# Kernel tuning notes

Measured on AMD Instinct MI355X. Metric: run time of the kernel, lower is better.

## Reference

```python
import jax, jax.numpy as jnp
import numpy as np

N_NODES = 20000
C_IN = 128
C_OUT = 128
C_MID = 8            # max(C_IN // 16, 8) per TP.__init__
NEIGHBOR_CG = 8
INF = 1000000.0
EPS = 1e-5
# real spherical harmonics for l=1 are ordered (m=-1,0,1) ~ (y,z,x)
P_L1 = jnp.array([[0., 1., 0.], [0., 0., 1.], [1., 0., 0.]], dtype=jnp.float32)


def equivariant_layer_norm(x, ln_w, ln_b):
    # x: (N, 4, C); l=0 block x[:, :1], l=1 block x[:, 1:4]
    x0 = x[:, :1, :]
    x0 = x0 - jnp.mean(x0, axis=-1, keepdims=True)          # mean only for l=0
    n0 = jnp.mean(jnp.sum(x0 * x0, axis=1, keepdims=True), axis=-1, keepdims=True)
    y0 = x0 * jax.lax.rsqrt(n0 + EPS) * ln_w[0] + ln_b
    x1 = x[:, 1:4, :]
    n1 = jnp.mean(jnp.sum(x1 * x1, axis=1, keepdims=True), axis=-1, keepdims=True)
    y1 = x1 * jax.lax.rsqrt(n1 + EPS) * ln_w[1]
    return jnp.concatenate([y0, y1], axis=1)


def rotation_to_z(vec):
    # vec: (..., 3) -> R with R @ unit(vec) = z_hat (Rodrigues, safe at c ~ -1)
    n = jnp.linalg.norm(vec, axis=-1, keepdims=True)
    v = vec / (n + 1e-9)
    c = v[..., 2]
    kx, ky = v[..., 1], -v[..., 0]                 # k = v x z_hat = (v_y, -v_x, 0)
    zero = jnp.zeros_like(kx)
    K = jnp.stack([
        jnp.stack([zero, zero, ky], -1),
        jnp.stack([zero, zero, -kx], -1),
        jnp.stack([-ky, kx, zero], -1)], -2)
    safe = c > -0.999
    denom = jnp.where(safe, 1.0 + c, 1.0)
    I = jnp.eye(3, dtype=vec.dtype)
    R = I + K + jnp.matmul(K, K) / denom[..., None, None]
    flip = jnp.array([[1., 0., 0.], [0., -1., 0.], [0., 0., -1.]], dtype=vec.dtype)
    return jnp.where(safe[..., None, None], R, flip)


def escn_tensor_product(msg, vec, so2_w0, so2_wr, so2_wi):
    # msg: (N, H, 4, Cm), vec: (N, H, 3)
    R = rotation_to_z(vec)                                      # (N,H,3,3)
    D1 = jnp.einsum('ij,nhjk,lk->nhil', P_L1, R, P_L1)          # Wigner-D, l=1
    l1 = jnp.einsum('nhij,nhjc->nhic', D1, msg[..., 1:4, :])    # rotate to edge frame
    # m = 0 channel mix across degrees (l=0 coeff, l=1 m=0 coeff)
    m0_in = jnp.stack([msg[..., 0, :], l1[..., 1, :]], axis=-2)  # (N,H,2,Cm)
    m0 = (m0_in.reshape(m0_in.shape[:-2] + (2 * C_MID,)) @ so2_w0).reshape(m0_in.shape)
    # m = +/-1 SO(2) convolution
    x_m1, x_p1 = l1[..., 0, :], l1[..., 2, :]
    y_p1 = x_p1 @ so2_wr - x_m1 @ so2_wi
    y_m1 = x_m1 @ so2_wr + x_p1 @ so2_wi
    out_l1 = jnp.stack([y_m1, m0[..., 1, :], y_p1], axis=-2)     # (N,H,3,Cm)
    out_l1 = jnp.einsum('nhji,nhjc->nhic', D1, out_l1)           # rotate back (D1^T)
    return jnp.concatenate([m0[..., :1, :], out_l1], axis=-2)    # (N,H,4,Cm)


def setup_inputs() -> dict:
    key = jax.random.key(0)
    ks = jax.random.split(key, 10)
    s_feats = jax.random.normal(ks[0], (N_NODES, 4, C_IN), jnp.float32)
    s_points = jax.random.normal(ks[1], (N_NODES, 3), jnp.float32) * 5.0
    neighbor_indices = jax.random.randint(ks[2], (N_NODES, 9), 0, N_NODES + 1)
    ln_w = 1.0 + 0.02 * jax.random.normal(ks[3], (2, C_IN), jnp.float32)
    ln_b = 0.02 * jax.random.normal(ks[4], (C_IN,), jnp.float32)
    w_in = jax.random.normal(ks[5], (2 * C_IN, C_MID), jnp.float32) / np.sqrt(2 * C_IN)
    w_out = jax.random.normal(ks[6], (C_MID, C_OUT), jnp.float32) / np.sqrt(C_MID)
    so2_w0 = jax.random.normal(ks[7], (2 * C_MID, 2 * C_MID), jnp.float32) / np.sqrt(2 * C_MID)
    so2_wr = jax.random.normal(ks[8], (C_MID, C_MID), jnp.float32) / np.sqrt(C_MID)
    so2_wi = jax.random.normal(ks[9], (C_MID, C_MID), jnp.float32) / np.sqrt(C_MID)
    return dict(s_feats=s_feats, s_points=s_points, neighbor_indices=neighbor_indices,
                ln_w=ln_w, ln_b=ln_b, w_in=w_in, w_out=w_out,
                so2_w0=so2_w0, so2_wr=so2_wr, so2_wi=so2_wi)


def reference(s_feats, s_points, neighbor_indices, ln_w, ln_b, w_in, w_out, so2_w0, so2_wr, so2_wi):
    N = s_feats.shape[0]
    x = equivariant_layer_norm(s_feats, ln_w, ln_b)                  # (N,4,C)
    sp_pad = jnp.concatenate([s_points, jnp.full((1, 3), INF, s_points.dtype)], 0)
    x_pad = jnp.concatenate([x, jnp.zeros_like(x[:1])], 0)
    idx = neighbor_indices[:, 1:]                                     # drop self
    mask = (idx < N).astype(x.dtype)                                  # (N,Hfull)
    npts = (sp_pad[idx] * mask[..., None])[:, :NEIGHBOR_CG]           # (N,H,3)
    nfts = (x_pad[idx] * mask[..., None, None])[:, :NEIGHBOR_CG]      # (N,H,4,C)
    vec = npts - s_points[:, None, :]                                 # (N,H,3)
    sfe = jnp.broadcast_to(x[:, None], nfts.shape)                    # (N,H,4,C)
    msg = jnp.concatenate([nfts, sfe], axis=-1) @ w_in                # (N,H,4,Cm)
    msg = escn_tensor_product(msg, vec, so2_w0, so2_wr, so2_wi)       # (N,H,4,Cm)
    out = msg.sum(axis=1) @ w_out                                     # (N,4,C_out)
    return out
```

## Files before the change

### kernel.cpp

```cpp
#include <hip/hip_runtime.h>
#include <math.h>

typedef float fx4 __attribute__((ext_vector_type(4)));
typedef float fx2 __attribute__((ext_vector_type(2)));

#define SWZ8(x)  __int_as_float(__builtin_amdgcn_ds_swizzle(__float_as_int(x), 0x201F))
#define SWZ16(x) __int_as_float(__builtin_amdgcn_ds_swizzle(__float_as_int(x), 0x401F))
#define SX32(x)  __shfl_xor((x), 32)

__global__ __launch_bounds__(256, 4) void k1_ln_proj(
    const float* __restrict__ s_feats,
    const float* __restrict__ ln_w,
    const float* __restrict__ ln_b,
    const float* __restrict__ w_in,
    float* __restrict__ ys,
    int N)
{
    const int lane = threadIdx.x & 63;
    const int kq = lane & 7;
    const int cg = lane >> 3;
    const int n = blockIdx.x * 4 + (threadIdx.x >> 6);

    float wa0[16], wa1[16], wb0[16], wb1[16];
    float B1 = 0.f, C1 = 0.f, B2 = 0.f, C2 = 0.f;
    #pragma unroll
    for (int t = 0; t < 16; t++) {
        int c = cg * 16 + t;
        float w1 = w_in[c * 8 + kq];
        float w2 = w_in[(128 + c) * 8 + kq];
        float l0 = ln_w[c], l1 = ln_w[128 + c], lb = ln_b[c];
        wa0[t] = w1 * l0; wa1[t] = w1 * l1;
        wb0[t] = w2 * l0; wb1[t] = w2 * l1;
        B1 += w1 * l0; C1 += lb * w1;
        B2 += w2 * l0; C2 += lb * w2;
    }
    B1 += SWZ8(B1);  C1 += SWZ8(C1);  B2 += SWZ8(B2);  C2 += SWZ8(C2);
    B1 += SWZ16(B1); C1 += SWZ16(C1); B2 += SWZ16(B2); C2 += SWZ16(C2);
    B1 += SX32(B1);  C1 += SX32(C1);  B2 += SX32(B2);  C2 += SX32(C2);

    if (n >= N) return;

    const float* sp = s_feats + (size_t)n * 512 + cg * 16;
    float accY[4] = {0.f, 0.f, 0.f, 0.f};
    float accS[4] = {0.f, 0.f, 0.f, 0.f};
    float ssum = 0.f, sq0 = 0.f, sq1 = 0.f;
    #pragma unroll
    for (int m = 0; m < 4; m++) {
        #pragma unroll
        for (int i = 0; i < 4; i++) {
            fx4 v = __builtin_nontemporal_load((const fx4*)(sp + m * 128 + i * 4));
            float e0 = v.x, e1 = v.y, e2 = v.z, e3 = v.w;
            if (m == 0) {
                accY[0] += e0 * wa0[i*4+0] + e1 * wa0[i*4+1] + e2 * wa0[i*4+2] + e3 * wa0[i*4+3];
                accS[0] += e0 * wb0[i*4+0] + e1 * wb0[i*4+1] + e2 * wb0[i*4+2] + e3 * wb0[i*4+3];
                ssum += e0 + e1 + e2 + e3;
                sq0  += e0 * e0 + e1 * e1 + e2 * e2 + e3 * e3;
            } else {
                accY[m] += e0 * wa1[i*4+0] + e1 * wa1[i*4+1] + e2 * wa1[i*4+2] + e3 * wa1[i*4+3];
                accS[m] += e0 * wb1[i*4+0] + e1 * wb1[i*4+1] + e2 * wb1[i*4+2] + e3 * wb1[i*4+3];
                sq1  += e0 * e0 + e1 * e1 + e2 * e2 + e3 * e3;
            }
        }
    }
    #define RED_ALL(FN) \
        accY[0] += FN(accY[0]); accY[1] += FN(accY[1]); accY[2] += FN(accY[2]); accY[3] += FN(accY[3]); \
        accS[0] += FN(accS[0]); accS[1] += FN(accS[1]); accS[2] += FN(accS[2]); accS[3] += FN(accS[3]); \
        ssum += FN(ssum); sq0 += FN(sq0); sq1 += FN(sq1);
    RED_ALL(SWZ8)
    RED_ALL(SWZ16)
    RED_ALL(SX32)
    #undef RED_ALL

    float mean = ssum * (1.0f / 128.0f);
    float r0 = rsqrtf((sq0 - ssum * mean) * (1.0f / 128.0f) + 1e-5f);
    float r1 = rsqrtf(sq1 * (1.0f / 128.0f) + 1e-5f);

    float aA = (cg & 2) ? ((cg & 1) ? accY[3] : accY[2]) : ((cg & 1) ? accY[1] : accY[0]);
    float aB = (cg & 2) ? ((cg & 1) ? accS[3] : accS[2]) : ((cg & 1) ? accS[1] : accS[0]);
    float av = (cg & 4) ? aB : aA;
    float Bv = (cg & 4) ? B2 : B1;
    float Cv = (cg & 4) ? C2 : C1;
    bool isM0 = (cg & 3) == 0;
    float outv = isM0 ? (r0 * (av - mean * Bv) + Cv) : (r1 * av);

    int src = ((lane >> 2) & 7) + ((lane & 3) << 3) + (lane & 32);
    float myv = __shfl(outv, src);
    ys[(size_t)n * 64 + lane] = myv;
}

#define TROW 40

__global__ __launch_bounds__(256, 4) void k2_edges(
    const float* __restrict__ ys,
    const float* __restrict__ s_points,
    const int*   __restrict__ nbr,
    const float* __restrict__ w0,
    const float* __restrict__ wr,
    const float* __restrict__ wi,
    const float* __restrict__ w_out,
    float* __restrict__ out,
    int N)
{
    __shared__ float tbuf[8][8 * TROW];
    __shared__ float abuf[8][32];

    const int tid = threadIdx.x;
    const int lane = tid & 63;
    const int h = lane >> 3, k = lane & 7;
    const int wv = tid >> 6;
    const int base = (blockIdx.x * 4 + wv) * 2;

    float c00[8], c08[8], c10[8], c18[8], cwr[8], cwi[8];
    #pragma unroll
    for (int j = 0; j < 8; j++) {
        c00[j] = w0[j * 16 + k];
        c08[j] = w0[(8 + j) * 16 + k];
        c10[j] = w0[j * 16 + 8 + k];
        c18[j] = w0[(8 + j) * 16 + 8 + k];
        cwr[j] = wr[j * 8 + k];
        cwi[j] = wi[j * 8 + k];
    }
    float wc0[8], wc1[8];
    #pragma unroll
    for (int kk = 0; kk < 8; kk++) {
        fx2 w2v = *(const fx2*)&w_out[kk * 128 + lane * 2];
        wc0[kk] = w2v.x; wc1[kk] = w2v.y;
    }

    if (base >= N) return;
    const int n1 = base + 1;
    const bool v1 = n1 < N;

    int idx0 = nbr[base * 9 + 1 + h];
    int idx1 = v1 ? nbr[n1 * 9 + 1 + h] : 0x7fffffff;
    bool mk0 = idx0 < N, mk1 = idx1 < N;

    float px0 = s_points[base * 3], py0 = s_points[base * 3 + 1], pz0 = s_points[base * 3 + 2];
    float px1 = v1 ? s_points[n1 * 3]     : 0.f;
    float py1 = v1 ? s_points[n1 * 3 + 1] : 0.f;
    float pz1 = v1 ? s_points[n1 * 3 + 2] : 0.f;
    float nx0 = mk0 ? s_points[idx0 * 3]     : 0.f;
    float ny0 = mk0 ? s_points[idx0 * 3 + 1] : 0.f;
    float nz0 = mk0 ? s_points[idx0 * 3 + 2] : 0.f;
    float nx1 = mk1 ? s_points[idx1 * 3]     : 0.f;
    float ny1 = mk1 ? s_points[idx1 * 3 + 1] : 0.f;
    float nz1 = mk1 ? s_points[idx1 * 3 + 2] : 0.f;
    fx4 yv0 = mk0 ? *(const fx4*)(ys + (size_t)idx0 * 64 + k * 4) : (fx4){0.f,0.f,0.f,0.f};
    fx4 yv1 = mk1 ? *(const fx4*)(ys + (size_t)idx1 * 64 + k * 4) : (fx4){0.f,0.f,0.f,0.f};
    fx4 sv0 = *(const fx4*)(ys + (size_t)base * 64 + 32 + k * 4);
    fx4 sv1 = v1 ? *(const fx4*)(ys + (size_t)n1 * 64 + 32 + k * 4) : (fx4){0.f,0.f,0.f,0.f};

    auto node_compute = [&](int slot, int nn, float PX, float PY, float PZ,
                            float NX, float NY, float NZ, fx4 YV, fx4 SV) {
        float vx = NX - PX, vy = NY - PY, vz = NZ - PZ;
        float nrm = sqrtf(vx * vx + vy * vy + vz * vz);
        float inv = 1.0f / (nrm + 1e-9f);
        float ux = vx * inv, uy = vy * inv, uz = vz * inv;
        float cz = uz;
        float kx = uy, ky = -ux;
        bool safe = cz > -0.999f;
        float idd = safe ? 1.0f / (1.0f + cz) : 1.0f;
        float D00, D01, D02, D10, D11, D12, D20, D21, D22;
        {
            float R00, R01, R02, R10, R11, R12, R20, R21, R22;
            if (safe) {
                R00 = 1.0f - ky * ky * idd; R01 = kx * ky * idd;        R02 = ky;
                R10 = kx * ky * idd;        R11 = 1.0f - kx * kx * idd; R12 = -kx;
                R20 = -ky;                  R21 = kx;                   R22 = 1.0f - (kx * kx + ky * ky) * idd;
            } else {
                R00 = 1.0f; R01 = 0.0f; R02 = 0.0f;
                R10 = 0.0f; R11 = -1.0f; R12 = 0.0f;
                R20 = 0.0f; R21 = 0.0f; R22 = -1.0f;
            }
            D00 = R11; D01 = R12; D02 = R10;
            D10 = R21; D11 = R22; D12 = R20;
            D20 = R01; D21 = R02; D22 = R00;
        }
        float msg0 = YV.x + SV.x, msg1 = YV.y + SV.y, msg2 = YV.z + SV.z, msg3 = YV.w + SV.w;
        float l1_0 = D00 * msg1 + D01 * msg2 + D02 * msg3;
        float l1_1 = D10 * msg1 + D11 * msg2 + D12 * msg3;
        float l1_2 = D20 * msg1 + D21 * msg2 + D22 * msg3;

        *(fx4*)&tbuf[slot][h * TROW + k * 4] = (fx4){msg0, l1_0, l1_1, l1_2};

        float m00 = 0.f, m01 = 0.f, ypl = 0.f, yml = 0.f;
        #pragma unroll
        for (int j = 0; j < 8; j++) {
            fx4 t = *(const fx4*)&tbuf[slot][h * TROW + j * 4];
            m00 += t.x * c00[j] + t.z * c08[j];
            m01 += t.x * c10[j] + t.z * c18[j];
            ypl += t.w * cwr[j] - t.y * cwi[j];
            yml += t.y * cwr[j] + t.w * cwi[j];
        }
        float f0 = m00;
        float f1 = D00 * yml + D10 * m01 + D20 * ypl;
        float f2 = D01 * yml + D11 * m01 + D21 * ypl;
        float f3 = D02 * yml + D12 * m01 + D22 * ypl;

        f0 += SWZ8(f0);  f1 += SWZ8(f1);  f2 += SWZ8(f2);  f3 += SWZ8(f3);
        f0 += SWZ16(f0); f1 += SWZ16(f1); f2 += SWZ16(f2); f3 += SWZ16(f3);
        f0 += SX32(f0);  f1 += SX32(f1);  f2 += SX32(f2);  f3 += SX32(f3);

        if (h == 0)
            *(fx4*)&abuf[slot][k * 4] = (fx4){f0, f1, f2, f3};

        float o0[4] = {0.f, 0.f, 0.f, 0.f}, o1[4] = {0.f, 0.f, 0.f, 0.f};
        #pragma unroll
        for (int kk = 0; kk < 8; kk++) {
            fx4 a = *(const fx4*)&abuf[slot][kk * 4];
            o0[0] += a.x * wc0[kk]; o1[0] += a.x * wc1[kk];
            o0[1] += a.y * wc0[kk]; o1[1] += a.y * wc1[kk];
            o0[2] += a.z * wc0[kk]; o1[2] += a.z * wc1[kk];
            o0[3] += a.w * wc0[kk]; o1[3] += a.w * wc1[kk];
        }
        float* op = out + (size_t)nn * 512;
        #pragma unroll
        for (int m = 0; m < 4; m++)
            *(fx2*)(op + m * 128 + lane * 2) = (fx2){o0[m], o1[m]};
    };

    node_compute(wv * 2 + 0, base, px0, py0, pz0, nx0, ny0, nz0, yv0, sv0);
    if (v1)
        node_compute(wv * 2 + 1, n1, px1, py1, pz1, nx1, ny1, nz1, yv1, sv1);
}

extern "C" void kernel_launch(void* const* d_in, const int* in_sizes, int n_in,
                              void* d_out, int out_size, void* d_ws, size_t ws_size,
                              hipStream_t stream) {
    const float* s_feats  = (const float*)d_in[0];
    const float* s_points = (const float*)d_in[1];
    const int*   nbr      = (const int*)d_in[2];
    const float* ln_w     = (const float*)d_in[3];
    const float* ln_b     = (const float*)d_in[4];
    const float* w_in     = (const float*)d_in[5];
    const float* w_out    = (const float*)d_in[6];
    const float* so2_w0   = (const float*)d_in[7];
    const float* so2_wr   = (const float*)d_in[8];
    const float* so2_wi   = (const float*)d_in[9];
    float* out = (float*)d_out;

    int N = in_sizes[0] / 512;
    float* ys = (float*)d_ws;

    int nb1 = (N + 3) / 4;
    int nb2 = (N + 7) / 8;
    k1_ln_proj<<<nb1, 256, 0, stream>>>(s_feats, ln_w, ln_b, w_in, ys, N);
    k2_edges<<<nb2, 256, 0, stream>>>(ys, s_points, nbr, so2_w0, so2_wr, so2_wi,
                                      w_out, out, N);
}
```

Before: 68.10 us.

## Process multiple nodes per wave in both kernels and vectorize output stores

Each wave in the layer-norm/projection kernel now handles five nodes, and each wave in the edge kernel handles eight nodes in pairs. The weight setup (w_in products and reductions, SO(2) and w_out weights) is amortized over more work and far fewer blocks are launched. The edge kernel loads w_out as fx4 and writes output with 128-bit stores split across half-waves. The first reduction step moves from a ds_swizzle to a DPP row operation. The trade-offs are fewer waves to hide gather latency and a lower occupancy hint on the edge kernel.

```diff
diff --git a/kernel.cpp b/kernel.cpp
--- a/kernel.cpp
+++ b/kernel.cpp
@@ -4,9 +4,15 @@
 typedef float fx4 __attribute__((ext_vector_type(4)));
 typedef float fx2 __attribute__((ext_vector_type(2)));
 
-#define SWZ8(x)  __int_as_float(__builtin_amdgcn_ds_swizzle(__float_as_int(x), 0x201F))
+__device__ __forceinline__ float DPP8(float x) {
+    int t = __builtin_amdgcn_update_dpp(0, __float_as_int(x), 0x128, 0xf, 0xf, false);
+    return __int_as_float(t);
+}
 #define SWZ16(x) __int_as_float(__builtin_amdgcn_ds_swizzle(__float_as_int(x), 0x401F))
 #define SX32(x)  __shfl_xor((x), 32)
+
+#define K1_NPW 5
+#define K2_NPW 8
 
 __global__ __launch_bounds__(256, 4) void k1_ln_proj(
     const float* __restrict__ s_feats,
@@ -19,7 +25,7 @@
     const int lane = threadIdx.x & 63;
     const int kq = lane & 7;
     const int cg = lane >> 3;
-    const int n = blockIdx.x * 4 + (threadIdx.x >> 6);
+    const int w = blockIdx.x * 4 + (threadIdx.x >> 6);
 
     float wa0[16], wa1[16], wb0[16], wb1[16];
     float B1 = 0.f, C1 = 0.f, B2 = 0.f, C2 = 0.f;
@@ -34,63 +40,68 @@
         B1 += w1 * l0; C1 += lb * w1;
         B2 += w2 * l0; C2 += lb * w2;
     }
-    B1 += SWZ8(B1);  C1 += SWZ8(C1);  B2 += SWZ8(B2);  C2 += SWZ8(C2);
+    B1 += DPP8(B1);  C1 += DPP8(C1);  B2 += DPP8(B2);  C2 += DPP8(C2);
     B1 += SWZ16(B1); C1 += SWZ16(C1); B2 += SWZ16(B2); C2 += SWZ16(C2);
     B1 += SX32(B1);  C1 += SX32(C1);  B2 += SX32(B2);  C2 += SX32(C2);
 
-    if (n >= N) return;
-
-    const float* sp = s_feats + (size_t)n * 512 + cg * 16;
-    float accY[4] = {0.f, 0.f, 0.f, 0.f};
-    float accS[4] = {0.f, 0.f, 0.f, 0.f};
-    float ssum = 0.f, sq0 = 0.f, sq1 = 0.f;
-    #pragma unroll
-    for (int m = 0; m < 4; m++) {
+    const int n0 = w * K1_NPW;
+    const int src = ((lane >> 2) & 7) + ((lane & 3) << 3) + (lane & 32);
+
+    #pragma unroll
+    for (int u = 0; u < K1_NPW; u++) {
+        int n = n0 + u;
+        if (n >= N) break;
+        const float* sp = s_feats + (size_t)n * 512 + cg * 16;
+        float accY[4] = {0.f, 0.f, 0.f, 0.f};
+        float accS[4] = {0.f, 0.f, 0.f, 0.f};
+        float ssum = 0.f, sq0 = 0.f, sq1 = 0.f;
         #pragma unroll
-        for (int i = 0; i < 4; i++) {
-            fx4 v = __builtin_nontemporal_load((const fx4*)(sp + m * 128 + i * 4));
-            float e0 = v.x, e1 = v.y, e2 = v.z, e3 = v.w;
-            if (m == 0) {
-                accY[0] += e0 * wa0[i*4+0] + e1 * wa0[i*4+1] + e2 * wa0[i*4+2] + e3 * wa0[i*4+3];
-                accS[0] += e0 * wb0[i*4+0] + e1 * wb0[i*4+1] + e2 * wb0[i*4+2] + e3 * wb0[i*4+3];
-                ssum += e0 + e1 + e2 + e3;
-                sq0  += e0 * e0 + e1 * e1 + e2 * e2 + e3 * e3;
-            } else {
-                accY[m] += e0 * wa1[i*4+0] + e1 * wa1[i*4+1] + e2 * wa1[i*4+2] + e3 * wa1[i*4+3];
-                accS[m] += e0 * wb1[i*4+0] + e1 * wb1[i*4+1] + e2 * wb1[i*4+2] + e3 * wb1[i*4+3];
-                sq1  += e0 * e0 + e1 * e1 + e2 * e2 + e3 * e3;
+        for (int m = 0; m < 4; m++) {
+            #pragma unroll
+            for (int i = 0; i < 4; i++) {
+                fx4 v = __builtin_nontemporal_load((const fx4*)(sp + m * 128 + i * 4));
+                float e0 = v.x, e1 = v.y, e2 = v.z, e3 = v.w;
+                if (m == 0) {
+                    accY[0] += e0 * wa0[i*4+0] + e1 * wa0[i*4+1] + e2 * wa0[i*4+2] + e3 * wa0[i*4+3];
+                    accS[0] += e0 * wb0[i*4+0] + e1 * wb0[i*4+1] + e2 * wb0[i*4+2] + e3 * wb0[i*4+3];
+                    ssum += e0 + e1 + e2 + e3;
+                    sq0  += e0 * e0 + e1 * e1 + e2 * e2 + e3 * e3;
+                } else {
+                    accY[m] += e0 * wa1[i*4+0] + e1 * wa1[i*4+1] + e2 * wa1[i*4+2] + e3 * wa1[i*4+3];
+                    accS[m] += e0 * wb1[i*4+0] + e1 * wb1[i*4+1] + e2 * wb1[i*4+2] + e3 * wb1[i*4+3];
+                    sq1  += e0 * e0 + e1 * e1 + e2 * e2 + e3 * e3;
+                }
             }
         }
-    }
-    #define RED_ALL(FN) \
-        accY[0] += FN(accY[0]); accY[1] += FN(accY[1]); accY[2] += FN(accY[2]); accY[3] += FN(accY[3]); \
-        accS[0] += FN(accS[0]); accS[1] += FN(accS[1]); accS[2] += FN(accS[2]); accS[3] += FN(accS[3]); \
-        ssum += FN(ssum); sq0 += FN(sq0); sq1 += FN(sq1);
-    RED_ALL(SWZ8)
-    RED_ALL(SWZ16)
-    RED_ALL(SX32)
-    #undef RED_ALL
-
-    float mean = ssum * (1.0f / 128.0f);
-    float r0 = rsqrtf((sq0 - ssum * mean) * (1.0f / 128.0f) + 1e-5f);
-    float r1 = rsqrtf(sq1 * (1.0f / 128.0f) + 1e-5f);
-
-    float aA = (cg & 2) ? ((cg & 1) ? accY[3] : accY[2]) : ((cg & 1) ? accY[1] : accY[0]);
-    float aB = (cg & 2) ? ((cg & 1) ? accS[3] : accS[2]) : ((cg & 1) ? accS[1] : accS[0]);
-    float av = (cg & 4) ? aB : aA;
-    float Bv = (cg & 4) ? B2 : B1;
-    float Cv = (cg & 4) ? C2 : C1;
-    bool isM0 = (cg & 3) == 0;
-    float outv = isM0 ? (r0 * (av - mean * Bv) + Cv) : (r1 * av);
-
-    int src = ((lane >> 2) & 7) + ((lane & 3) << 3) + (lane & 32);
-    float myv = __shfl(outv, src);
-    ys[(size_t)n * 64 + lane] = myv;
+        #define RED_ALL(FN) \
+            accY[0] += FN(accY[0]); accY[1] += FN(accY[1]); accY[2] += FN(accY[2]); accY[3] += FN(accY[3]); \
+            accS[0] += FN(accS[0]); accS[1] += FN(accS[1]); accS[2] += FN(accS[2]); accS[3] += FN(accS[3]); \
+            ssum += FN(ssum); sq0 += FN(sq0); sq1 += FN(sq1);
+        RED_ALL(DPP8)
+        RED_ALL(SWZ16)
+        RED_ALL(SX32)
+        #undef RED_ALL
+
+        float mean = ssum * (1.0f / 128.0f);
+        float r0 = rsqrtf((sq0 - ssum * mean) * (1.0f / 128.0f) + 1e-5f);
+        float r1 = rsqrtf(sq1 * (1.0f / 128.0f) + 1e-5f);
+
+        float aA = (cg & 2) ? ((cg & 1) ? accY[3] : accY[2]) : ((cg & 1) ? accY[1] : accY[0]);
+        float aB = (cg & 2) ? ((cg & 1) ? accS[3] : accS[2]) : ((cg & 1) ? accS[1] : accS[0]);
+        float av = (cg & 4) ? aB : aA;
+        float Bv = (cg & 4) ? B2 : B1;
+        float Cv = (cg & 4) ? C2 : C1;
+        bool isM0 = (cg & 3) == 0;
+        float outv = isM0 ? (r0 * (av - mean * Bv) + Cv) : (r1 * av);
+
+        float myv = __shfl(outv, src);
+        ys[(size_t)n * 64 + lane] = myv;
+    }
 }
 
 #define TROW 40
 
-__global__ __launch_bounds__(256, 4) void k2_edges(
+__global__ __launch_bounds__(256, 3) void k2_edges(
     const float* __restrict__ ys,
     const float* __restrict__ s_points,
     const int*   __restrict__ nbr,
@@ -108,7 +119,8 @@
     const int lane = tid & 63;
     const int h = lane >> 3, k = lane & 7;
     const int wv = tid >> 6;
-    const int base = (blockIdx.x * 4 + wv) * 2;
+    const int w = blockIdx.x * 4 + wv;
+    const int base = w * K2_NPW;
 
     float c00[8], c08[8], c10[8], c18[8], cwr[8], cwi[8];
     #pragma unroll
@@ -120,35 +132,14 @@
         cwr[j] = wr[j * 8 + k];
         cwi[j] = wi[j * 8 + k];
     }
-    float wc0[8], wc1[8];
-    #pragma unroll
-    for (int kk = 0; kk < 8; kk++) {
-        fx2 w2v = *(const fx2*)&w_out[kk * 128 + lane * 2];
-        wc0[kk] = w2v.x; wc1[kk] = w2v.y;
-    }
+    const int c0 = 4 * (lane & 31);
+    const bool hi = lane >= 32;
+    fx4 wo[8];
+    #pragma unroll
+    for (int kk = 0; kk < 8; kk++)
+        wo[kk] = *(const fx4*)&w_out[kk * 128 + c0];
 
     if (base >= N) return;
-    const int n1 = base + 1;
-    const bool v1 = n1 < N;
-
-    int idx0 = nbr[base * 9 + 1 + h];
-    int idx1 = v1 ? nbr[n1 * 9 + 1 + h] : 0x7fffffff;
-    bool mk0 = idx0 < N, mk1 = idx1 < N;
-
-    float px0 = s_points[base * 3], py0 = s_points[base * 3 + 1], pz0 = s_points[base * 3 + 2];
-    float px1 = v1 ? s_points[n1 * 3]     : 0.f;
-    float py1 = v1 ? s_points[n1 * 3 + 1] : 0.f;
-    float pz1 = v1 ? s_points[n1 * 3 + 2] : 0.f;
-    float nx0 = mk0 ? s_points[idx0 * 3]     : 0.f;
-    float ny0 = mk0 ? s_points[idx0 * 3 + 1] : 0.f;
-    float nz0 = mk0 ? s_points[idx0 * 3 + 2] : 0.f;
-    float nx1 = mk1 ? s_points[idx1 * 3]     : 0.f;
-    float ny1 = mk1 ? s_points[idx1 * 3 + 1] : 0.f;
-    float nz1 = mk1 ? s_points[idx1 * 3 + 2] : 0.f;
-    fx4 yv0 = mk0 ? *(const fx4*)(ys + (size_t)idx0 * 64 + k * 4) : (fx4){0.f,0.f,0.f,0.f};
-    fx4 yv1 = mk1 ? *(const fx4*)(ys + (size_t)idx1 * 64 + k * 4) : (fx4){0.f,0.f,0.f,0.f};
-    fx4 sv0 = *(const fx4*)(ys + (size_t)base * 64 + 32 + k * 4);
-    fx4 sv1 = v1 ? *(const fx4*)(ys + (size_t)n1 * 64 + 32 + k * 4) : (fx4){0.f,0.f,0.f,0.f};
 
     auto node_compute = [&](int slot, int nn, float PX, float PY, float PZ,
                             float NX, float NY, float NZ, fx4 YV, fx4 SV) {
@@ -197,31 +188,57 @@
         float f2 = D01 * yml + D11 * m01 + D21 * ypl;
         float f3 = D02 * yml + D12 * m01 + D22 * ypl;
 
-        f0 += SWZ8(f0);  f1 += SWZ8(f1);  f2 += SWZ8(f2);  f3 += SWZ8(f3);
+        f0 += DPP8(f0);  f1 += DPP8(f1);  f2 += DPP8(f2);  f3 += DPP8(f3);
         f0 += SWZ16(f0); f1 += SWZ16(f1); f2 += SWZ16(f2); f3 += SWZ16(f3);
         f0 += SX32(f0);  f1 += SX32(f1);  f2 += SX32(f2);  f3 += SX32(f3);
 
         if (h == 0)
             *(fx4*)&abuf[slot][k * 4] = (fx4){f0, f1, f2, f3};
 
-        float o0[4] = {0.f, 0.f, 0.f, 0.f}, o1[4] = {0.f, 0.f, 0.f, 0.f};
+        fx4 olo = {0.f, 0.f, 0.f, 0.f}, ohi = {0.f, 0.f, 0.f, 0.f};
         #pragma unroll
         for (int kk = 0; kk < 8; kk++) {
             fx4 a = *(const fx4*)&abuf[slot][kk * 4];
-            o0[0] += a.x * wc0[kk]; o1[0] += a.x * wc1[kk];
-            o0[1] += a.y * wc0[kk]; o1[1] += a.y * wc1[kk];
-            o0[2] += a.z * wc0[kk]; o1[2] += a.z * wc1[kk];
-            o0[3] += a.w * wc0[kk]; o1[3] += a.w * wc1[kk];
-        }
-        float* op = out + (size_t)nn * 512;
-        #pragma unroll
-        for (int m = 0; m < 4; m++)
-            *(fx2*)(op + m * 128 + lane * 2) = (fx2){o0[m], o1[m]};
+            float am0 = hi ? a.z : a.x;
+            float am1 = hi ? a.w : a.y;
+            olo += am0 * wo[kk];
+            ohi += am1 * wo[kk];
+        }
+        float* op = out + (size_t)nn * 512 + (hi ? 256 : 0);
+        *(fx4*)(op + c0)       = olo;
+        *(fx4*)(op + 128 + c0) = ohi;
     };
 
-    node_compute(wv * 2 + 0, base, px0, py0, pz0, nx0, ny0, nz0, yv0, sv0);
-    if (v1)
-        node_compute(wv * 2 + 1, n1, px1, py1, pz1, nx1, ny1, nz1, yv1, sv1);
+    #pragma unroll
+    for (int p = 0; p < K2_NPW / 2; p++) {
+        int n0 = base + 2 * p;
+        if (n0 >= N) break;
+        int n1 = n0 + 1;
+        bool v1 = n1 < N;
+
+        int idx0 = nbr[n0 * 9 + 1 + h];
+        int idx1 = v1 ? nbr[n1 * 9 + 1 + h] : 0x7fffffff;
+        bool mk0 = idx0 < N, mk1 = idx1 < N;
+
+        float px0 = s_points[n0 * 3], py0 = s_points[n0 * 3 + 1], pz0 = s_points[n0 * 3 + 2];
+        float px1 = v1 ? s_points[n1 * 3]     : 0.f;
+        float py1 = v1 ? s_points[n1 * 3 + 1] : 0.f;
+        float pz1 = v1 ? s_points[n1 * 3 + 2] : 0.f;
+        float nx0 = mk0 ? s_points[idx0 * 3]     : 0.f;
+        float ny0 = mk0 ? s_points[idx0 * 3 + 1] : 0.f;
+        float nz0 = mk0 ? s_points[idx0 * 3 + 2] : 0.f;
+        float nx1 = mk1 ? s_points[idx1 * 3]     : 0.f;
+        float ny1 = mk1 ? s_points[idx1 * 3 + 1] : 0.f;
+        float nz1 = mk1 ? s_points[idx1 * 3 + 2] : 0.f;
+        fx4 yv0 = mk0 ? *(const fx4*)(ys + (size_t)idx0 * 64 + k * 4) : (fx4){0.f,0.f,0.f,0.f};
+        fx4 yv1 = mk1 ? *(const fx4*)(ys + (size_t)idx1 * 64 + k * 4) : (fx4){0.f,0.f,0.f,0.f};
+        fx4 sv0 = *(const fx4*)(ys + (size_t)n0 * 64 + 32 + k * 4);
+        fx4 sv1 = v1 ? *(const fx4*)(ys + (size_t)n1 * 64 + 32 + k * 4) : (fx4){0.f,0.f,0.f,0.f};
+
+        node_compute(wv * 2 + 0, n0, px0, py0, pz0, nx0, ny0, nz0, yv0, sv0);
+        if (v1)
+            node_compute(wv * 2 + 1, n1, px1, py1, pz1, nx1, ny1, nz1, yv1, sv1);
+    }
 }
 
 extern "C" void kernel_launch(void* const* d_in, const int* in_sizes, int n_in,
@@ -242,8 +259,8 @@
     int N = in_sizes[0] / 512;
     float* ys = (float*)d_ws;
 
-    int nb1 = (N + 3) / 4;
-    int nb2 = (N + 7) / 8;
+    int nb1 = (N + 4 * K1_NPW - 1) / (4 * K1_NPW);
+    int nb2 = (N + 4 * K2_NPW - 1) / (4 * K2_NPW);
     k1_ln_proj<<<nb1, 256, 0, stream>>>(s_feats, ln_w, ln_b, w_in, ys, N);
     k2_edges<<<nb2, 256, 0, stream>>>(ys, s_points, nbr, so2_w0, so2_wr, so2_wi,
                                       w_out, out, N);
```

Measured after the change: 85.13 us. +25.0%, slower.
